# Performance work log

Measured on AMD Instinct MI355X. Metric: run time of the kernel, lower is better.

## Reference

```python
import jax, jax.numpy as jnp
import numpy as np

NEG_SLOPE = 0.2
N_NODES = 50000


def gatv2_layer(x, src, dst, Wl, Wr, att, b, concat):
    # GATv2Conv (PyG semantics): x_l = lin_l(x) feeds messages (source side),
    # x_r = lin_r(x) is the target side; attention logit per edge/head is
    # att . leaky_relu(x_l[src] + x_r[dst]); softmax over incoming edges of dst.
    H, C = att.shape
    n = x.shape[0]
    xl = (x @ Wl).reshape(n, H, C)   # [N,H,C]
    xr = (x @ Wr).reshape(n, H, C)
    h = xl[src] + xr[dst]            # [E,H,C] gather
    logits = jnp.einsum('ehc,hc->eh', jax.nn.leaky_relu(h, NEG_SLOPE), att)  # [E,H]
    # segment softmax over target nodes
    m = jax.ops.segment_max(logits, dst, num_segments=n)
    m = jnp.where(jnp.isfinite(m), m, 0.0)
    ex = jnp.exp(logits - m[dst])
    s = jax.ops.segment_sum(ex, dst, num_segments=n)
    alpha = ex / (s[dst] + 1e-16)    # [E,H]
    msg = xl[src] * alpha[:, :, None]               # [E,H,C]
    out = jax.ops.segment_sum(msg, dst, num_segments=n)  # [N,H,C] scatter-add
    out = out.reshape(n, H * C) if concat else out.mean(axis=1)
    return out + b


def setup_inputs() -> dict:
    key = jax.random.key(0)
    ks = jax.random.split(key, 10)
    in_c, out_c, heads = 128, 64, 2
    node_fts = jax.random.normal(ks[0], (N_NODES, in_c), dtype=jnp.float32)
    edge_index = jax.random.randint(ks[1], (2, 800000), 0, N_NODES, dtype=jnp.int64)
    sc = 0.1
    return {
        'node_fts': node_fts,
        'edge_index': edge_index,
        'Wl1': jax.random.normal(ks[2], (in_c, heads * out_c), dtype=jnp.float32) * sc,
        'Wr1': jax.random.normal(ks[3], (in_c, heads * out_c), dtype=jnp.float32) * sc,
        'att1': jax.random.normal(ks[4], (heads, out_c), dtype=jnp.float32) * sc,
        'b1': jnp.zeros((heads * out_c,), dtype=jnp.float32),
        'Wl2': jax.random.normal(ks[5], (heads * out_c, out_c), dtype=jnp.float32) * sc,
        'Wr2': jax.random.normal(ks[6], (heads * out_c, out_c), dtype=jnp.float32) * sc,
        'att2': jax.random.normal(ks[7], (1, out_c), dtype=jnp.float32) * sc,
        'b2': jnp.zeros((out_c,), dtype=jnp.float32),
    }


def reference(node_fts, edge_index, Wl1, Wr1, att1, b1, Wl2, Wr2, att2, b2):
    n = node_fts.shape[0]
    loop = jnp.arange(n, dtype=edge_index.dtype)  # add_self_loops=True default
    src = jnp.concatenate([edge_index[0], loop])
    dst = jnp.concatenate([edge_index[1], loop])
    x = gatv2_layer(node_fts, src, dst, Wl1, Wr1, att1, b1, concat=True)
    x = jax.nn.relu(x)
    x = gatv2_layer(x, src, dst, Wl2, Wr2, att2, b2, concat=False)
    x = jax.nn.relu(x)
    return x
```

## Files before the change

### kernel.cpp

```cpp
#include <hip/hip_runtime.h>
#include <math.h>

typedef unsigned short ush;
typedef short bf16x8 __attribute__((ext_vector_type(8)));
typedef float f32x4 __attribute__((ext_vector_type(4)));
typedef ush ushx8 __attribute__((ext_vector_type(8)));

__device__ __forceinline__ ush f2bf(float f) {
    unsigned u = __float_as_uint(f);
    u += 0x7FFFu + ((u >> 16) & 1u);
    return (ush)(u >> 16);
}
__device__ __forceinline__ float bf2f(ush u) {
    return __uint_as_float((unsigned)u << 16);
}

__global__ __launch_bounds__(256) void prep_x_k(const float* __restrict__ x,
                                                ush* __restrict__ hi,
                                                ush* __restrict__ lo, int tot4) {
    for (int i = blockIdx.x * blockDim.x + threadIdx.x; i < tot4;
         i += gridDim.x * blockDim.x) {
        const float4 v = reinterpret_cast<const float4*>(x)[i];
        ushort4 h, l4;
        h.x = f2bf(v.x); l4.x = f2bf(v.x - bf2f(h.x));
        h.y = f2bf(v.y); l4.y = f2bf(v.y - bf2f(h.y));
        h.z = f2bf(v.z); l4.z = f2bf(v.z - bf2f(h.z));
        h.w = f2bf(v.w); l4.w = f2bf(v.w - bf2f(h.w));
        reinterpret_cast<ushort4*>(hi)[i] = h;
        reinterpret_cast<ushort4*>(lo)[i] = l4;
    }
}

__global__ __launch_bounds__(64) void prep_w_k(
    const float* __restrict__ Wl1, const float* __restrict__ Wr1,
    const float* __restrict__ Wl2, const float* __restrict__ Wr2,
    ush* __restrict__ wph, ush* __restrict__ wpl) {
    const int bid = blockIdx.x, l = threadIdx.x;
    const float* W;
    int C, fid;
    if (bid < 32)      { W = Wl1; C = 128; fid = bid; }
    else if (bid < 64) { W = Wr1; C = 128; fid = bid - 32; }
    else if (bid < 80) { W = Wl2; C = 64;  fid = bid - 64; }
    else               { W = Wr2; C = 64;  fid = bid - 80; }
    const int nc16 = C / 16;
    const int ks = fid / nc16, c16 = fid % nc16;
#pragma unroll
    for (int j = 0; j < 8; ++j) {
        const int k = ks * 32 + (l >> 4) * 8 + j;
        const int c = c16 * 16 + (l & 15);
        const float v = W[(size_t)k * C + c];
        const ush h = f2bf(v);
        wph[(size_t)(bid * 64 + l) * 8 + j] = h;
        wpl[(size_t)(bid * 64 + l) * 8 + j] = f2bf(v - bf2f(h));
    }
}

template <int CW>
__global__ __launch_bounds__(256) void gemm_mfma_k(
    const ush* __restrict__ xhi, const ush* __restrict__ xlo,
    const ush* __restrict__ wh1, const ush* __restrict__ wl1,
    const ush* __restrict__ wh2, const ush* __restrict__ wl2,
    ush* __restrict__ ybf, float* __restrict__ yf, int n) {
    constexpr int NC16 = CW / 16;
    constexpr int SPW = CW / 64;
    const int l = threadIdx.x & 63;
    const int w = threadIdx.x >> 6;
    const int r0 = blockIdx.x * 64 + w * 16;
    const int slab = blockIdx.y;
    const bool isW1 = slab < SPW;
    const int slab_local = isW1 ? slab : slab - SPW;
    const ush* __restrict__ wh = isW1 ? wh1 : wh2;
    const ush* __restrict__ wl = isW1 ? wl1 : wl2;

    const int arow = min(r0 + (l & 15), n - 1);
    const int kb = (l >> 4) * 8;
    bf16x8 ah[4], al[4];
#pragma unroll
    for (int ks = 0; ks < 4; ++ks) {
        ah[ks] = *reinterpret_cast<const bf16x8*>(xhi + (size_t)arow * 128 + ks * 32 + kb);
        al[ks] = *reinterpret_cast<const bf16x8*>(xlo + (size_t)arow * 128 + ks * 32 + kb);
    }
    const int drow = (l >> 4) * 4;
    const int dcol = l & 15;
#pragma unroll
    for (int c16 = 0; c16 < 4; ++c16) {
        f32x4 acc = {0.f, 0.f, 0.f, 0.f};
#pragma unroll
        for (int ks = 0; ks < 4; ++ks) {
            const int fid = ks * NC16 + slab_local * 4 + c16;
            const bf16x8 bh = *reinterpret_cast<const bf16x8*>(wh + (size_t)(fid * 64 + l) * 8);
            const bf16x8 bl = *reinterpret_cast<const bf16x8*>(wl + (size_t)(fid * 64 + l) * 8);
            acc = __builtin_amdgcn_mfma_f32_16x16x32_bf16(ah[ks], bh, acc, 0, 0, 0);
            acc = __builtin_amdgcn_mfma_f32_16x16x32_bf16(al[ks], bh, acc, 0, 0, 0);
            acc = __builtin_amdgcn_mfma_f32_16x16x32_bf16(ah[ks], bl, acc, 0, 0, 0);
        }
        const int cg = slab_local * 64 + c16 * 16 + dcol;
#pragma unroll
        for (int q = 0; q < 4; ++q) {
            const int gr = r0 + drow + q;
            if (gr < n) {
                if (isW1) ybf[(size_t)gr * CW + cg] = f2bf(acc[q]);
                else      yf[(size_t)gr * CW + cg] = acc[q];
            }
        }
    }
}

__global__ __launch_bounds__(256) void hist_k(const int* __restrict__ dsts,
                                              int* __restrict__ ghist,
                                              int e0, int etot) {
    __shared__ int h[512];
    const int t = threadIdx.x;
    for (int i = t; i < 512; i += 256) h[i] = 0;
    __syncthreads();
    for (int i = blockIdx.x * blockDim.x + t; i < etot; i += gridDim.x * blockDim.x) {
        const int d = (i < e0) ? dsts[i] : (i - e0);
        atomicAdd(&h[d >> 7], 1);
    }
    __syncthreads();
    for (int i = t; i < 512; i += 256)
        if (h[i]) atomicAdd(&ghist[i], h[i]);
}

__global__ __launch_bounds__(512) void scanb_k(const int* __restrict__ ghist,
                                               int* __restrict__ boff,
                                               int* __restrict__ cur) {
    __shared__ int red[512];
    const int t = threadIdx.x;
    const int x = ghist[t];
    red[t] = x;
    __syncthreads();
#pragma unroll
    for (int s = 1; s < 512; s <<= 1) {
        const int add = (t >= s) ? red[t - s] : 0;
        __syncthreads();
        red[t] += add;
        __syncthreads();
    }
    const int excl = red[t] - x;
    boff[t] = excl;
    cur[t] = excl;
}

__global__ __launch_bounds__(256) void semisort_k(
    const int* __restrict__ srcs, const int* __restrict__ dsts,
    int* __restrict__ cur, int2* __restrict__ pairs, int e0, int etot) {
    __shared__ int hist[512], gbase[512], lcur[512];
    const int t = threadIdx.x;
    const int start = blockIdx.x * 2048;
    const int end = min(start + 2048, etot);
    for (int i = t; i < 512; i += 256) { hist[i] = 0; lcur[i] = 0; }
    __syncthreads();
    for (int i = start + t; i < end; i += 256) {
        const int d = (i < e0) ? dsts[i] : (i - e0);
        atomicAdd(&hist[d >> 7], 1);
    }
    __syncthreads();
    for (int i = t; i < 512; i += 256) {
        const int c = hist[i];
        gbase[i] = c ? atomicAdd(&cur[i], c) : 0;
    }
    __syncthreads();
    for (int i = start + t; i < end; i += 256) {
        int s, d;
        if (i < e0) { s = srcs[i]; d = dsts[i]; } else { s = d = i - e0; }
        const int b = d >> 7;
        const int p = atomicAdd(&lcur[b], 1);
        int2 pr; pr.x = s; pr.y = d;
        pairs[gbase[b] + p] = pr;
    }
}

__global__ __launch_bounds__(256) void bucket_fill_k(
    const int2* __restrict__ pairs, const int* __restrict__ boff,
    int* __restrict__ row_ptr, int* __restrict__ csr_src, int n, int etot) {
    __shared__ int cnt[128], cur[128];
    const int b = blockIdx.x, t = threadIdx.x;
    const int lo = boff[b], hi = boff[b + 1];
    if (t < 128) cnt[t] = 0;
    __syncthreads();
    for (int e = lo + t; e < hi; e += 256)
        atomicAdd(&cnt[pairs[e].y & 127], 1);
    __syncthreads();
    const int x = (t < 128) ? cnt[t] : 0;
#pragma unroll
    for (int s = 1; s < 128; s <<= 1) {
        const int add = (t < 128 && t >= s) ? cnt[t - s] : 0;
        __syncthreads();
        if (t < 128) cnt[t] += add;
        __syncthreads();
    }
    if (t < 128) {
        const int excl = cnt[t] - x;
        cur[t] = excl;
        const int d = b * 128 + t;
        if (d < n) row_ptr[d] = lo + excl;
    }
    if (b == 0 && t == 0) row_ptr[n] = etot;
    __syncthreads();
    for (int e = lo + t; e < hi; e += 256) {
        const int2 p = pairs[e];
        const int pos = atomicAdd(&cur[p.y & 127], 1);
        csr_src[lo + pos] = p.x;
    }
}

__global__ __launch_bounds__(256) void deg_hist_k(const int* __restrict__ row_ptr,
                                                  int* __restrict__ dbin, int n) {
    __shared__ int h[128];
    const int t = threadIdx.x;
    if (t < 128) h[t] = 0;
    __syncthreads();
    const int d = blockIdx.x * 256 + t;
    if (d < n) {
        const int deg = row_ptr[d + 1] - row_ptr[d];
        atomicAdd(&h[127 - min(deg, 127)], 1);
    }
    __syncthreads();
    if (t < 128 && h[t]) atomicAdd(&dbin[t], h[t]);
}

__global__ __launch_bounds__(128) void deg_scan_k(const int* __restrict__ dbin,
                                                  int* __restrict__ dcur) {
    __shared__ int red[128];
    const int t = threadIdx.x;
    const int x = dbin[t];
    red[t] = x;
    __syncthreads();
#pragma unroll
    for (int s = 1; s < 128; s <<= 1) {
        const int add = (t >= s) ? red[t - s] : 0;
        __syncthreads();
        red[t] += add;
        __syncthreads();
    }
    dcur[t] = red[t] - x;
}

__global__ __launch_bounds__(256) void deg_scatter_k(const int* __restrict__ row_ptr,
                                                     int* __restrict__ dcur,
                                                     int* __restrict__ order, int n) {
    __shared__ int h[128], gbase[128], lcur[128];
    const int t = threadIdx.x;
    if (t < 128) { h[t] = 0; lcur[t] = 0; }
    __syncthreads();
    const int d = blockIdx.x * 256 + t;
    int bin = -1;
    if (d < n) {
        const int deg = row_ptr[d + 1] - row_ptr[d];
        bin = 127 - min(deg, 127);
        atomicAdd(&h[bin], 1);
    }
    __syncthreads();
    if (t < 128) gbase[t] = h[t] ? atomicAdd(&dcur[t], h[t]) : 0;
    __syncthreads();
    if (d < n) {
        const int p = atomicAdd(&lcur[bin], 1);
        order[gbase[bin] + p] = d;
    }
}

__global__ __launch_bounds__(256) void gat_dst2_k(
    const ush* __restrict__ xl, const float* __restrict__ xr,
    const int* __restrict__ row_ptr, const int* __restrict__ csr_src,
    const int* __restrict__ order, const float* __restrict__ att,
    const float* __restrict__ bias, ush* __restrict__ h1hi,
    ush* __restrict__ h1lo, int n) {
    const int lane = threadIdx.x & 63;
    const int g = lane >> 4, il = lane & 15;
    const int w = (blockIdx.x * blockDim.x + threadIdx.x) >> 6;
    if (w >= n) return;
    const int d = order[w];

    float xv[8], av[8];
    {
        const float4* xp = reinterpret_cast<const float4*>(xr + (size_t)d * 128 + il * 8);
        const float4* ap = reinterpret_cast<const float4*>(att + il * 8);
        const float4 x0 = xp[0], x1 = xp[1], a0 = ap[0], a1 = ap[1];
        xv[0]=x0.x; xv[1]=x0.y; xv[2]=x0.z; xv[3]=x0.w;
        xv[4]=x1.x; xv[5]=x1.y; xv[6]=x1.z; xv[7]=x1.w;
        av[0]=a0.x; av[1]=a0.y; av[2]=a0.z; av[3]=a0.w;
        av[4]=a1.x; av[5]=a1.y; av[6]=a1.z; av[7]=a1.w;
    }
    const int rp0 = row_ptr[d], rp1 = row_ptr[d + 1];

    float s = 0.f;
    float acc[8] = {0.f, 0.f, 0.f, 0.f, 0.f, 0.f, 0.f, 0.f};
    int i = rp0 + g;
    for (; i + 4 < rp1; i += 8) {
        const int s0 = csr_src[i];
        const int s1 = csr_src[i + 4];
        const ushx8 u0 = *reinterpret_cast<const ushx8*>(xl + (((size_t)(unsigned)s0) << 7) + il * 8);
        const ushx8 u1 = *reinterpret_cast<const ushx8*>(xl + (((size_t)(unsigned)s1) << 7) + il * 8);
        float f0[8], f1[8], p0 = 0.f, p1 = 0.f;
#pragma unroll
        for (int j = 0; j < 8; ++j) {
            f0[j] = bf2f((ush)u0[j]);
            const float v = f0[j] + xv[j];
            p0 = fmaf(av[j], fmaxf(v, 0.2f * v), p0);
        }
#pragma unroll
        for (int j = 0; j < 8; ++j) {
            f1[j] = bf2f((ush)u1[j]);
            const float v = f1[j] + xv[j];
            p1 = fmaf(av[j], fmaxf(v, 0.2f * v), p1);
        }
        p0 += __shfl_xor(p0, 4, 64); p0 += __shfl_xor(p0, 2, 64); p0 += __shfl_xor(p0, 1, 64);
        p1 += __shfl_xor(p1, 4, 64); p1 += __shfl_xor(p1, 2, 64); p1 += __shfl_xor(p1, 1, 64);
        const float w0 = __expf(p0), w1 = __expf(p1);
        s += w0 + w1;
#pragma unroll
        for (int j = 0; j < 8; ++j) acc[j] = fmaf(w0, f0[j], fmaf(w1, f1[j], acc[j]));
    }
    if (i < rp1) {
        const int s0 = csr_src[i];
        const ushx8 u0 = *reinterpret_cast<const ushx8*>(xl + (((size_t)(unsigned)s0) << 7) + il * 8);
        float f0[8], p0 = 0.f;
#pragma unroll
        for (int j = 0; j < 8; ++j) {
            f0[j] = bf2f((ush)u0[j]);
            const float v = f0[j] + xv[j];
            p0 = fmaf(av[j], fmaxf(v, 0.2f * v), p0);
        }
        p0 += __shfl_xor(p0, 4, 64); p0 += __shfl_xor(p0, 2, 64); p0 += __shfl_xor(p0, 1, 64);
        const float w0 = __expf(p0);
        s += w0;
#pragma unroll
        for (int j = 0; j < 8; ++j) acc[j] = fmaf(w0, f0[j], acc[j]);
    }
#pragma unroll
    for (int off = 16; off <= 32; off <<= 1) {
        s += __shfl_xor(s, off, 64);
#pragma unroll
        for (int j = 0; j < 8; ++j) acc[j] += __shfl_xor(acc[j], off, 64);
    }
    if (g == 0) {
        const float inv = 1.f / (s + 1e-16f);
        float bv[8];
        {
            const float4* bp = reinterpret_cast<const float4*>(bias + il * 8);
            const float4 b0 = bp[0], b1 = bp[1];
            bv[0]=b0.x; bv[1]=b0.y; bv[2]=b0.z; bv[3]=b0.w;
            bv[4]=b1.x; bv[5]=b1.y; bv[6]=b1.z; bv[7]=b1.w;
        }
        ushx8 hh, ll;
#pragma unroll
        for (int j = 0; j < 8; ++j) {
            const float o = fmaxf(fmaf(acc[j], inv, bv[j]), 0.f);
            const ush h = f2bf(o);
            hh[j] = h;
            ll[j] = f2bf(o - bf2f(h));
        }
        *reinterpret_cast<ushx8*>(h1hi + (size_t)d * 128 + il * 8) = hh;
        *reinterpret_cast<ushx8*>(h1lo + (size_t)d * 128 + il * 8) = ll;
    }
}

__global__ __launch_bounds__(256) void gat_dst1_k(
    const ush* __restrict__ xl, const float* __restrict__ xr,
    const int* __restrict__ row_ptr, const int* __restrict__ csr_src,
    const int* __restrict__ order, const float* __restrict__ att,
    const float* __restrict__ bias, float* __restrict__ out, int n) {
    const int lane = threadIdx.x & 63;
    const int g = lane >> 3, il = lane & 7;
    const int w = (blockIdx.x * blockDim.x + threadIdx.x) >> 6;
    if (w >= n) return;
    const int d = order[w];

    float xv[8], av[8];
    {
        const float4* xp = reinterpret_cast<const float4*>(xr + (size_t)d * 64 + il * 8);
        const float4* ap = reinterpret_cast<const float4*>(att + il * 8);
        const float4 x0 = xp[0], x1 = xp[1], a0 = ap[0], a1 = ap[1];
        xv[0]=x0.x; xv[1]=x0.y; xv[2]=x0.z; xv[3]=x0.w;
        xv[4]=x1.x; xv[5]=x1.y; xv[6]=x1.z; xv[7]=x1.w;
        av[0]=a0.x; av[1]=a0.y; av[2]=a0.z; av[3]=a0.w;
        av[4]=a1.x; av[5]=a1.y; av[6]=a1.z; av[7]=a1.w;
    }
    const int rp0 = row_ptr[d], rp1 = row_ptr[d + 1];

    float s = 0.f;
    float acc[8] = {0.f, 0.f, 0.f, 0.f, 0.f, 0.f, 0.f, 0.f};
    int i = rp0 + g;
    for (; i + 8 < rp1; i += 16) {
        const int s0 = csr_src[i];
        const int s1 = csr_src[i + 8];
        const ushx8 u0 = *reinterpret_cast<const ushx8*>(xl + (((size_t)(unsigned)s0) << 6) + il * 8);
        const ushx8 u1 = *reinterpret_cast<const ushx8*>(xl + (((size_t)(unsigned)s1) << 6) + il * 8);
        float f0[8], f1[8], p0 = 0.f, p1 = 0.f;
#pragma unroll
        for (int j = 0; j < 8; ++j) {
            f0[j] = bf2f((ush)u0[j]);
            const float v = f0[j] + xv[j];
            p0 = fmaf(av[j], fmaxf(v, 0.2f * v), p0);
        }
#pragma unroll
        for (int j = 0; j < 8; ++j) {
            f1[j] = bf2f((ush)u1[j]);
            const float v = f1[j] + xv[j];
            p1 = fmaf(av[j], fmaxf(v, 0.2f * v), p1);
        }
        p0 += __shfl_xor(p0, 4, 64); p0 += __shfl_xor(p0, 2, 64); p0 += __shfl_xor(p0, 1, 64);
        p1 += __shfl_xor(p1, 4, 64); p1 += __shfl_xor(p1, 2, 64); p1 += __shfl_xor(p1, 1, 64);
        const float w0 = __expf(p0), w1 = __expf(p1);
        s += w0 + w1;
#pragma unroll
        for (int j = 0; j < 8; ++j) acc[j] = fmaf(w0, f0[j], fmaf(w1, f1[j], acc[j]));
    }
    if (i < rp1) {
        const int s0 = csr_src[i];
        const ushx8 u0 = *reinterpret_cast<const ushx8*>(xl + (((size_t)(unsigned)s0) << 6) + il * 8);
        float f0[8], p0 = 0.f;
#pragma unroll
        for (int j = 0; j < 8; ++j) {
            f0[j] = bf2f((ush)u0[j]);
            const float v = f0[j] + xv[j];
            p0 = fmaf(av[j], fmaxf(v, 0.2f * v), p0);
        }
        p0 += __shfl_xor(p0, 4, 64); p0 += __shfl_xor(p0, 2, 64); p0 += __shfl_xor(p0, 1, 64);
        const float w0 = __expf(p0);
        s += w0;
#pragma unroll
        for (int j = 0; j < 8; ++j) acc[j] = fmaf(w0, f0[j], acc[j]);
    }
#pragma unroll
    for (int off = 8; off <= 32; off <<= 1) {
        s += __shfl_xor(s, off, 64);
#pragma unroll
        for (int j = 0; j < 8; ++j) acc[j] += __shfl_xor(acc[j], off, 64);
    }
    if (g == 0) {
        const float inv = 1.f / (s + 1e-16f);
        float bv[8];
        {
            const float4* bp = reinterpret_cast<const float4*>(bias + il * 8);
            const float4 b0 = bp[0], b1 = bp[1];
            bv[0]=b0.x; bv[1]=b0.y; bv[2]=b0.z; bv[3]=b0.w;
            bv[4]=b1.x; bv[5]=b1.y; bv[6]=b1.z; bv[7]=b1.w;
        }
        float4 o0, o1;
        o0.x = fmaxf(fmaf(acc[0], inv, bv[0]), 0.f);
        o0.y = fmaxf(fmaf(acc[1], inv, bv[1]), 0.f);
        o0.z = fmaxf(fmaf(acc[2], inv, bv[2]), 0.f);
        o0.w = fmaxf(fmaf(acc[3], inv, bv[3]), 0.f);
        o1.x = fmaxf(fmaf(acc[4], inv, bv[4]), 0.f);
        o1.y = fmaxf(fmaf(acc[5], inv, bv[5]), 0.f);
        o1.z = fmaxf(fmaf(acc[6], inv, bv[6]), 0.f);
        o1.w = fmaxf(fmaf(acc[7], inv, bv[7]), 0.f);
        float4* op = reinterpret_cast<float4*>(out + (size_t)d * 64 + il * 8);
        op[0] = o0;
        op[1] = o1;
    }
}

extern "C" void kernel_launch(void* const* d_in, const int* in_sizes, int n_in,
                              void* d_out, int out_size, void* d_ws, size_t ws_size,
                              hipStream_t stream) {
    const float* x    = (const float*)d_in[0];
    const int*   ei   = (const int*)d_in[1];
    const float* Wl1  = (const float*)d_in[2];
    const float* Wr1  = (const float*)d_in[3];
    const float* att1 = (const float*)d_in[4];
    const float* b1   = (const float*)d_in[5];
    const float* Wl2  = (const float*)d_in[6];
    const float* Wr2  = (const float*)d_in[7];
    const float* att2 = (const float*)d_in[8];
    const float* b2   = (const float*)d_in[9];

    const int n    = in_sizes[0] / 128;
    const int e0   = in_sizes[1] / 2;
    const int etot = e0 + n;
    const int* srcs = ei;
    const int* dsts = ei + e0;

    float* ws = (float*)d_ws;
    ush*   xhi  = (ush*)ws;
    ush*   xlo  = (ush*)(ws + (size_t)n * 64);
    ush*   xlbf = (ush*)(ws + (size_t)n * 128);
    float* xr   = ws + (size_t)n * 192;
    int* row_ptr = (int*)(ws + (size_t)n * 320);
    int* ghist   = row_ptr + (n + 2);
    int* dbin    = ghist + 512;
    int* dcur    = dbin + 128;
    int* boff    = dcur + 128;
    int* cur     = boff + 512;
    int* order   = cur + 512;
    int* csr_src = order + n;
    int2* pairs  = (int2*)(csr_src + etot);
    ush* wph     = (ush*)(pairs + etot);
    ush* wpl     = wph + 96 * 512;

    const int NB  = (n + 127) / 128;
    const int NDB = (n + 255) / 256;
    const int nblka = (etot + 2047) / 2048;

    hipMemsetAsync(ghist, 0, 640 * sizeof(int), stream);
    hist_k<<<256, 256, 0, stream>>>(dsts, ghist, e0, etot);
    scanb_k<<<1, 512, 0, stream>>>(ghist, boff, cur);
    semisort_k<<<nblka, 256, 0, stream>>>(srcs, dsts, cur, pairs, e0, etot);
    bucket_fill_k<<<NB, 256, 0, stream>>>(pairs, boff, row_ptr, csr_src, n, etot);

    deg_hist_k<<<NDB, 256, 0, stream>>>(row_ptr, dbin, n);
    deg_scan_k<<<1, 128, 0, stream>>>(dbin, dcur);
    deg_scatter_k<<<NDB, 256, 0, stream>>>(row_ptr, dcur, order, n);

    prep_w_k<<<96, 64, 0, stream>>>(Wl1, Wr1, Wl2, Wr2, wph, wpl);
    prep_x_k<<<2048, 256, 0, stream>>>(x, xhi, xlo, n * 32);

    const int gx = (n + 63) / 64;

    gemm_mfma_k<128><<<dim3(gx, 4), 256, 0, stream>>>(
        xhi, xlo, wph, wpl, wph + 32 * 512, wpl + 32 * 512, xlbf, xr, n);
    gat_dst2_k<<<(n + 3) / 4, 256, 0, stream>>>(xlbf, xr, row_ptr, csr_src, order,
                                                att1, b1, xhi, xlo, n);

    gemm_mfma_k<64><<<dim3(gx, 2), 256, 0, stream>>>(
        xhi, xlo, wph + 64 * 512, wpl + 64 * 512, wph + 80 * 512, wpl + 80 * 512,
        xlbf, xr, n);
    gat_dst1_k<<<(n + 3) / 4, 256, 0, stream>>>(xlbf, xr, row_ptr, csr_src, order,
                                                att2, b2, (float*)d_out, n);
}
```

Baseline: 202.8 us.

## Fuse input bf16 split into GEMM1, pack edge pairs, merge degree histogram

Removes the separate prep_x kernel by converting fp32 node features to hi/lo bf16 inside the first GEMM. Each GEMM block now computes all output column slabs from one A-tile load instead of launching one grid row per slab. Edge pairs are packed into a single int (source in the low 24 bits, local destination in the high bits), which halves semisort traffic. The degree histogram is folded into bucket_fill, dropping a kernel launch and a row_ptr pass. The cost is less grid parallelism in the GEMMs and a limit of 2^24 on node ids.

Measured after the change: 188.0 us, median of 2. 7.3% less time.

```diff
diff --git a/kernel.cpp b/kernel.cpp
--- a/kernel.cpp
+++ b/kernel.cpp
@@ -13,22 +13,6 @@
 }
 __device__ __forceinline__ float bf2f(ush u) {
     return __uint_as_float((unsigned)u << 16);
-}
-
-__global__ __launch_bounds__(256) void prep_x_k(const float* __restrict__ x,
-                                                ush* __restrict__ hi,
-                                                ush* __restrict__ lo, int tot4) {
-    for (int i = blockIdx.x * blockDim.x + threadIdx.x; i < tot4;
-         i += gridDim.x * blockDim.x) {
-        const float4 v = reinterpret_cast<const float4*>(x)[i];
-        ushort4 h, l4;
-        h.x = f2bf(v.x); l4.x = f2bf(v.x - bf2f(h.x));
-        h.y = f2bf(v.y); l4.y = f2bf(v.y - bf2f(h.y));
-        h.z = f2bf(v.z); l4.z = f2bf(v.z - bf2f(h.z));
-        h.w = f2bf(v.w); l4.w = f2bf(v.w - bf2f(h.w));
-        reinterpret_cast<ushort4*>(hi)[i] = h;
-        reinterpret_cast<ushort4*>(lo)[i] = l4;
-    }
 }
 
 __global__ __launch_bounds__(64) void prep_w_k(
@@ -55,52 +39,106 @@
     }
 }
 
-template <int CW>
-__global__ __launch_bounds__(256) void gemm_mfma_k(
-    const ush* __restrict__ xhi, const ush* __restrict__ xlo,
+__global__ __launch_bounds__(256) void gemm1_k(
+    const float* __restrict__ x,
     const ush* __restrict__ wh1, const ush* __restrict__ wl1,
     const ush* __restrict__ wh2, const ush* __restrict__ wl2,
     ush* __restrict__ ybf, float* __restrict__ yf, int n) {
-    constexpr int NC16 = CW / 16;
-    constexpr int SPW = CW / 64;
     const int l = threadIdx.x & 63;
     const int w = threadIdx.x >> 6;
     const int r0 = blockIdx.x * 64 + w * 16;
-    const int slab = blockIdx.y;
-    const bool isW1 = slab < SPW;
-    const int slab_local = isW1 ? slab : slab - SPW;
-    const ush* __restrict__ wh = isW1 ? wh1 : wh2;
-    const ush* __restrict__ wl = isW1 ? wl1 : wl2;
-
+    const int arow = min(r0 + (l & 15), n - 1);
+    const int kb = (l >> 4) * 8;
+
+    bf16x8 ah[4], al[4];
+#pragma unroll
+    for (int ks = 0; ks < 4; ++ks) {
+        const float* ap = x + (size_t)arow * 128 + ks * 32 + kb;
+        const float4 v0 = *reinterpret_cast<const float4*>(ap);
+        const float4 v1 = *reinterpret_cast<const float4*>(ap + 4);
+        const float fv[8] = {v0.x, v0.y, v0.z, v0.w, v1.x, v1.y, v1.z, v1.w};
+#pragma unroll
+        for (int j = 0; j < 8; ++j) {
+            const ush h = f2bf(fv[j]);
+            ah[ks][j] = (short)h;
+            al[ks][j] = (short)f2bf(fv[j] - bf2f(h));
+        }
+    }
+    const int drow = (l >> 4) * 4;
+    const int dcol = l & 15;
+#pragma unroll
+    for (int slab = 0; slab < 4; ++slab) {
+        const bool isW1 = slab < 2;
+        const int sl = slab & 1;
+        const ush* __restrict__ wh = isW1 ? wh1 : wh2;
+        const ush* __restrict__ wl = isW1 ? wl1 : wl2;
+#pragma unroll
+        for (int c16 = 0; c16 < 4; ++c16) {
+            f32x4 acc = {0.f, 0.f, 0.f, 0.f};
+#pragma unroll
+            for (int ks = 0; ks < 4; ++ks) {
+                const int fid = ks * 8 + sl * 4 + c16;
+                const bf16x8 bh = *reinterpret_cast<const bf16x8*>(wh + (size_t)(fid * 64 + l) * 8);
+                const bf16x8 bl = *reinterpret_cast<const bf16x8*>(wl + (size_t)(fid * 64 + l) * 8);
+                acc = __builtin_amdgcn_mfma_f32_16x16x32_bf16(ah[ks], bh, acc, 0, 0, 0);
+                acc = __builtin_amdgcn_mfma_f32_16x16x32_bf16(al[ks], bh, acc, 0, 0, 0);
+                acc = __builtin_amdgcn_mfma_f32_16x16x32_bf16(ah[ks], bl, acc, 0, 0, 0);
+            }
+            const int cg = sl * 64 + c16 * 16 + dcol;
+#pragma unroll
+            for (int q = 0; q < 4; ++q) {
+                const int gr = r0 + drow + q;
+                if (gr < n) {
+                    if (isW1) ybf[(size_t)gr * 128 + cg] = f2bf(acc[q]);
+                    else      yf[(size_t)gr * 128 + cg] = acc[q];
+                }
+            }
+        }
+    }
+}
+
+__global__ __launch_bounds__(256) void gemm2_k(
+    const ush* __restrict__ ahi, const ush* __restrict__ alo,
+    const ush* __restrict__ whl, const ush* __restrict__ wll,
+    const ush* __restrict__ whr, const ush* __restrict__ wlr,
+    ush* __restrict__ ybf, float* __restrict__ yf, int n) {
+    const int l = threadIdx.x & 63;
+    const int w = threadIdx.x >> 6;
+    const int r0 = blockIdx.x * 64 + w * 16;
     const int arow = min(r0 + (l & 15), n - 1);
     const int kb = (l >> 4) * 8;
     bf16x8 ah[4], al[4];
 #pragma unroll
     for (int ks = 0; ks < 4; ++ks) {
-        ah[ks] = *reinterpret_cast<const bf16x8*>(xhi + (size_t)arow * 128 + ks * 32 + kb);
-        al[ks] = *reinterpret_cast<const bf16x8*>(xlo + (size_t)arow * 128 + ks * 32 + kb);
+        ah[ks] = *reinterpret_cast<const bf16x8*>(ahi + (size_t)arow * 128 + ks * 32 + kb);
+        al[ks] = *reinterpret_cast<const bf16x8*>(alo + (size_t)arow * 128 + ks * 32 + kb);
     }
     const int drow = (l >> 4) * 4;
     const int dcol = l & 15;
 #pragma unroll
-    for (int c16 = 0; c16 < 4; ++c16) {
-        f32x4 acc = {0.f, 0.f, 0.f, 0.f};
-#pragma unroll
-        for (int ks = 0; ks < 4; ++ks) {
-            const int fid = ks * NC16 + slab_local * 4 + c16;
-            const bf16x8 bh = *reinterpret_cast<const bf16x8*>(wh + (size_t)(fid * 64 + l) * 8);
-            const bf16x8 bl = *reinterpret_cast<const bf16x8*>(wl + (size_t)(fid * 64 + l) * 8);
-            acc = __builtin_amdgcn_mfma_f32_16x16x32_bf16(ah[ks], bh, acc, 0, 0, 0);
-            acc = __builtin_amdgcn_mfma_f32_16x16x32_bf16(al[ks], bh, acc, 0, 0, 0);
-            acc = __builtin_amdgcn_mfma_f32_16x16x32_bf16(ah[ks], bl, acc, 0, 0, 0);
-        }
-        const int cg = slab_local * 64 + c16 * 16 + dcol;
-#pragma unroll
-        for (int q = 0; q < 4; ++q) {
-            const int gr = r0 + drow + q;
-            if (gr < n) {
-                if (isW1) ybf[(size_t)gr * CW + cg] = f2bf(acc[q]);
-                else      yf[(size_t)gr * CW + cg] = acc[q];
+    for (int slab = 0; slab < 2; ++slab) {
+        const ush* __restrict__ wh = slab ? whr : whl;
+        const ush* __restrict__ wl = slab ? wlr : wll;
+#pragma unroll
+        for (int c16 = 0; c16 < 4; ++c16) {
+            f32x4 acc = {0.f, 0.f, 0.f, 0.f};
+#pragma unroll
+            for (int ks = 0; ks < 4; ++ks) {
+                const int fid = ks * 4 + c16;
+                const bf16x8 bh = *reinterpret_cast<const bf16x8*>(wh + (size_t)(fid * 64 + l) * 8);
+                const bf16x8 bl = *reinterpret_cast<const bf16x8*>(wl + (size_t)(fid * 64 + l) * 8);
+                acc = __builtin_amdgcn_mfma_f32_16x16x32_bf16(ah[ks], bh, acc, 0, 0, 0);
+                acc = __builtin_amdgcn_mfma_f32_16x16x32_bf16(al[ks], bh, acc, 0, 0, 0);
+                acc = __builtin_amdgcn_mfma_f32_16x16x32_bf16(ah[ks], bl, acc, 0, 0, 0);
+            }
+            const int cg = c16 * 16 + dcol;
+#pragma unroll
+            for (int q = 0; q < 4; ++q) {
+                const int gr = r0 + drow + q;
+                if (gr < n) {
+                    if (slab == 0) ybf[(size_t)gr * 64 + cg] = f2bf(acc[q]);
+                    else           yf[(size_t)gr * 64 + cg] = acc[q];
+                }
             }
         }
     }
@@ -144,7 +182,7 @@
 
 __global__ __launch_bounds__(256) void semisort_k(
     const int* __restrict__ srcs, const int* __restrict__ dsts,
-    int* __restrict__ cur, int2* __restrict__ pairs, int e0, int etot) {
+    int* __restrict__ cur, int* __restrict__ pairs, int e0, int etot) {
     __shared__ int hist[512], gbase[512], lcur[512];
     const int t = threadIdx.x;
     const int start = blockIdx.x * 2048;
@@ -166,21 +204,21 @@
         if (i < e0) { s = srcs[i]; d = dsts[i]; } else { s = d = i - e0; }
         const int b = d >> 7;
         const int p = atomicAdd(&lcur[b], 1);
-        int2 pr; pr.x = s; pr.y = d;
-        pairs[gbase[b] + p] = pr;
+        pairs[gbase[b] + p] = s | ((d & 127) << 24);
     }
 }
 
 __global__ __launch_bounds__(256) void bucket_fill_k(
-    const int2* __restrict__ pairs, const int* __restrict__ boff,
-    int* __restrict__ row_ptr, int* __restrict__ csr_src, int n, int etot) {
-    __shared__ int cnt[128], cur[128];
+    const int* __restrict__ pairs, const int* __restrict__ boff,
+    int* __restrict__ row_ptr, int* __restrict__ csr_src,
+    int* __restrict__ dbin, int n, int etot) {
+    __shared__ int cnt[128], cur[128], hd[128];
     const int b = blockIdx.x, t = threadIdx.x;
     const int lo = boff[b], hi = boff[b + 1];
-    if (t < 128) cnt[t] = 0;
+    if (t < 128) { cnt[t] = 0; hd[t] = 0; }
     __syncthreads();
     for (int e = lo + t; e < hi; e += 256)
-        atomicAdd(&cnt[pairs[e].y & 127], 1);
+        atomicAdd(&cnt[(pairs[e] >> 24) & 127], 1);
     __syncthreads();
     const int x = (t < 128) ? cnt[t] : 0;
 #pragma unroll
@@ -194,30 +232,19 @@
         const int excl = cnt[t] - x;
         cur[t] = excl;
         const int d = b * 128 + t;
-        if (d < n) row_ptr[d] = lo + excl;
+        if (d < n) {
+            row_ptr[d] = lo + excl;
+            atomicAdd(&hd[127 - min(x, 127)], 1);
+        }
     }
     if (b == 0 && t == 0) row_ptr[n] = etot;
     __syncthreads();
+    if (t < 128 && hd[t]) atomicAdd(&dbin[t], hd[t]);
     for (int e = lo + t; e < hi; e += 256) {
-        const int2 p = pairs[e];
-        const int pos = atomicAdd(&cur[p.y & 127], 1);
-        csr_src[lo + pos] = p.x;
-    }
-}
-
-__global__ __launch_bounds__(256) void deg_hist_k(const int* __restrict__ row_ptr,
-                                                  int* __restrict__ dbin, int n) {
-    __shared__ int h[128];
-    const int t = threadIdx.x;
-    if (t < 128) h[t] = 0;
-    __syncthreads();
-    const int d = blockIdx.x * 256 + t;
-    if (d < n) {
-        const int deg = row_ptr[d + 1] - row_ptr[d];
-        atomicAdd(&h[127 - min(deg, 127)], 1);
-    }
-    __syncthreads();
-    if (t < 128 && h[t]) atomicAdd(&dbin[t], h[t]);
+        const int p = pairs[e];
+        const int pos = atomicAdd(&cur[(p >> 24) & 127], 1);
+        csr_src[lo + pos] = p & 0xFFFFFF;
+    }
 }
 
 __global__ __launch_bounds__(128) void deg_scan_k(const int* __restrict__ dbin,
@@ -474,8 +501,8 @@
     const int* dsts = ei + e0;
 
     float* ws = (float*)d_ws;
-    ush*   xhi  = (ush*)ws;
-    ush*   xlo  = (ush*)(ws + (size_t)n * 64);
+    ush*   h1hi = (ush*)ws;
+    ush*   h1lo = (ush*)(ws + (size_t)n * 64);
     ush*   xlbf = (ush*)(ws + (size_t)n * 128);
     float* xr   = ws + (size_t)n * 192;
     int* row_ptr = (int*)(ws + (size_t)n * 320);
@@ -486,7 +513,7 @@
     int* cur     = boff + 512;
     int* order   = cur + 512;
     int* csr_src = order + n;
-    int2* pairs  = (int2*)(csr_src + etot);
+    int* pairs   = csr_src + etot;
     ush* wph     = (ush*)(pairs + etot);
     ush* wpl     = wph + 96 * 512;
 
@@ -498,25 +525,21 @@
     hist_k<<<256, 256, 0, stream>>>(dsts, ghist, e0, etot);
     scanb_k<<<1, 512, 0, stream>>>(ghist, boff, cur);
     semisort_k<<<nblka, 256, 0, stream>>>(srcs, dsts, cur, pairs, e0, etot);
-    bucket_fill_k<<<NB, 256, 0, stream>>>(pairs, boff, row_ptr, csr_src, n, etot);
-
-    deg_hist_k<<<NDB, 256, 0, stream>>>(row_ptr, dbin, n);
+    bucket_fill_k<<<NB, 256, 0, stream>>>(pairs, boff, row_ptr, csr_src, dbin, n, etot);
     deg_scan_k<<<1, 128, 0, stream>>>(dbin, dcur);
     deg_scatter_k<<<NDB, 256, 0, stream>>>(row_ptr, dcur, order, n);
 
     prep_w_k<<<96, 64, 0, stream>>>(Wl1, Wr1, Wl2, Wr2, wph, wpl);
-    prep_x_k<<<2048, 256, 0, stream>>>(x, xhi, xlo, n * 32);
 
     const int gx = (n + 63) / 64;
 
-    gemm_mfma_k<128><<<dim3(gx, 4), 256, 0, stream>>>(
-        xhi, xlo, wph, wpl, wph + 32 * 512, wpl + 32 * 512, xlbf, xr, n);
+    gemm1_k<<<gx, 256, 0, stream>>>(x, wph, wpl, wph + 32 * 512, wpl + 32 * 512,
+                                    xlbf, xr, n);
     gat_dst2_k<<<(n + 3) / 4, 256, 0, stream>>>(xlbf, xr, row_ptr, csr_src, order,
-                                                att1, b1, xhi, xlo, n);
-
-    gemm_mfma_k<64><<<dim3(gx, 2), 256, 0, stream>>>(
-        xhi, xlo, wph + 64 * 512, wpl + 64 * 512, wph + 80 * 512, wpl + 80 * 512,
-        xlbf, xr, n);
+                                                att1, b1, h1hi, h1lo, n);
+
+    gemm2_k<<<gx, 256, 0, stream>>>(h1hi, h1lo, wph + 64 * 512, wpl + 64 * 512,
+                                    wph + 80 * 512, wpl + 80 * 512, xlbf, xr, n);
     gat_dst1_k<<<(n + 3) / 4, 256, 0, stream>>>(xlbf, xr, row_ptr, csr_src, order,
                                                 att2, b2, (float*)d_out, n);
 }
```
